# Optimization experiments

Measured on AMD Instinct MI355X. Metric: run time of the kernel, lower is better.

The kernel has to match this reference:

```python
import jax, jax.numpy as jnp
import numpy as np

N_HEAD = 16
D_MODEL = 1024
T_DIM = 64
# Faithful to torch source: temperature = d_model // n_head ** 0.5  ==  d_model // (n_head**0.5)
TEMPERATURE = D_MODEL // (N_HEAD ** 0.5)  # 1024 // 4.0 = 256.0
LN_EPS = 1e-5


def setup_inputs() -> dict:
    key = jax.random.key(0)
    ks = jax.random.split(key, 10)
    B, S = 4, 2048
    w = 0.02  # weight scale to keep activations/logits in a sane range
    return {
        "q": jax.random.normal(ks[0], (B, S, D_MODEL), jnp.float32),
        "k": jax.random.normal(ks[1], (B, S, D_MODEL), jnp.float32),
        "v": jax.random.normal(ks[2], (B, S, D_MODEL), jnp.float32),
        "t": jax.random.normal(ks[3], (B, T_DIM), jnp.float32),
        "w_q": jax.random.normal(ks[4], (D_MODEL, D_MODEL), jnp.float32) * w,
        "w_k": jax.random.normal(ks[5], (D_MODEL, D_MODEL), jnp.float32) * w,
        "w_v": jax.random.normal(ks[6], (D_MODEL, D_MODEL), jnp.float32) * w,
        "w_fc": jax.random.normal(ks[7], (D_MODEL, D_MODEL), jnp.float32) * w,
        "ada_w": jax.random.normal(ks[8], (2 * D_MODEL, T_DIM), jnp.float32) * w,
        "ada_b": jax.random.normal(ks[9], (2 * D_MODEL,), jnp.float32) * w,
    }


def _ada_layer_norm(x, t_emb, ada_w, ada_b):
    # linear(gelu(t_emb)) -> [B, 2*d]; exact (erf) GELU as in torch nn.GELU default
    emb = jax.nn.gelu(t_emb, approximate=False) @ ada_w.T + ada_b
    emb = emb[:, None, :]  # [B, 1, 2*d]
    scale, shift = jnp.split(emb, 2, axis=-1)
    mean = jnp.mean(x, axis=-1, keepdims=True)
    var = jnp.var(x, axis=-1, keepdims=True)
    ln = (x - mean) * jax.lax.rsqrt(var + LN_EPS)
    return ln * (1.0 + scale) + shift


def reference(q, k, v, t, w_q, w_k, w_v, w_fc, ada_w, ada_b):
    B, Sq, D = q.shape
    Sk = k.shape[1]
    H, Dk = N_HEAD, D // N_HEAD

    q = _ada_layer_norm(q, t, ada_w, ada_b)
    residual = q

    # projections (torch Linear, no bias): y = x @ W.T
    qh = (q @ w_q.T).reshape(B, Sq, H, Dk).transpose(0, 2, 1, 3)  # [B,H,Sq,Dk]
    kh = (k @ w_k.T).reshape(B, Sk, H, Dk).transpose(0, 2, 1, 3)
    vh = (v @ w_v.T).reshape(B, Sk, H, Dk).transpose(0, 2, 1, 3)

    scores = jnp.einsum("bhqd,bhkd->bhqk", qh, kh) / TEMPERATURE
    attn = jax.nn.softmax(scores, axis=-1)
    out = jnp.einsum("bhqk,bhkd->bhqd", attn, vh)  # [B,H,Sq,Dk]

    out = out.transpose(0, 2, 1, 3).reshape(B, Sq, D)
    out = out @ w_fc.T  # dropout is identity in eval
    return out + residual
```

## Files before the change

### kernel.cpp

```cpp
#include <hip/hip_runtime.h>
#include <hip/hip_bf16.h>
#include <cstdint>

typedef short bf16x8 __attribute__((ext_vector_type(8)));
typedef float f32x4  __attribute__((ext_vector_type(4)));
typedef unsigned short u16x8 __attribute__((ext_vector_type(8)));
typedef unsigned short u16x4 __attribute__((ext_vector_type(4)));

#define SEQ    2048
#define BATCH  4
#define DMODEL 1024
#define NHEAD  16
#define DKH    64
#define MROWS  (BATCH * SEQ)

__device__ __forceinline__ unsigned short f2bf(float f) {
  union { float f; uint32_t u; } x; x.f = f;
  uint32_t r = (x.u + 0x7fffu + ((x.u >> 16) & 1u)) >> 16;
  return (unsigned short)r;
}
__device__ __forceinline__ float bf2f(unsigned short u) {
  union { uint32_t u; float f; } x; x.u = ((uint32_t)u) << 16;
  return x.f;
}
__device__ __forceinline__ uint32_t pack_bf2(float lo, float hi) {
  uint32_t r;
  asm("v_cvt_pk_bf16_f32 %0, %1, %2" : "=v"(r) : "v"(lo), "v"(hi));
  return r;
}
__device__ __forceinline__ void gload_lds16(const void* g, void* l) {
  __builtin_amdgcn_global_load_lds(
      (const __attribute__((address_space(1))) void*)g,
      (__attribute__((address_space(3))) void*)l, 16, 0, 0);
}

__global__ __launch_bounds__(256) void cast4_kernel(
    const float* __restrict__ s0, const float* __restrict__ s1,
    const float* __restrict__ s2, const float* __restrict__ s3,
    unsigned short* __restrict__ d0, unsigned short* __restrict__ d1,
    unsigned short* __restrict__ d2, unsigned short* __restrict__ d3) {
  int z = blockIdx.y;
  const float* in = z == 0 ? s0 : z == 1 ? s1 : z == 2 ? s2 : s3;
  unsigned short* out = z == 0 ? d0 : z == 1 ? d1 : z == 2 ? d2 : d3;
  int i = (blockIdx.x * 256 + threadIdx.x) * 4;
  float4 v = *(const float4*)(in + i);
  u16x4 o;
  o[0] = f2bf(v.x); o[1] = f2bf(v.y); o[2] = f2bf(v.z); o[3] = f2bf(v.w);
  *(u16x4*)(out + i) = o;
}

__global__ __launch_bounds__(256) void cast2_kernel(
    const float* __restrict__ s0, const float* __restrict__ s1,
    unsigned short* __restrict__ d0, unsigned short* __restrict__ d1) {
  int z = blockIdx.y;
  const float* in = z == 0 ? s0 : s1;
  unsigned short* out = z == 0 ? d0 : d1;
  int i = (blockIdx.x * 256 + threadIdx.x) * 4;
  float4 v = *(const float4*)(in + i);
  u16x4 o;
  o[0] = f2bf(v.x); o[1] = f2bf(v.y); o[2] = f2bf(v.z); o[3] = f2bf(v.w);
  *(u16x4*)(out + i) = o;
}

__global__ __launch_bounds__(256) void ada_emb_kernel(
    const float* __restrict__ t, const float* __restrict__ ada_w,
    const float* __restrict__ ada_b, float* __restrict__ emb) {
  int b = blockIdx.y;
  int j = blockIdx.x * 256 + threadIdx.x;
  __shared__ float g[64];
  if (threadIdx.x < 64) {
    float x = t[b * 64 + threadIdx.x];
    g[threadIdx.x] = x * 0.5f * (1.0f + erff(x * 0.70710678118654752f));
  }
  __syncthreads();
  float acc = ada_b[j];
  const float* wr = ada_w + (size_t)j * 64;
  #pragma unroll
  for (int i = 0; i < 64; ++i) acc += g[i] * wr[i];
  emb[b * 2048 + j] = acc;
}

__global__ __launch_bounds__(256) void adaln_kernel(
    const float* __restrict__ q, const float* __restrict__ emb,
    unsigned short* __restrict__ xbf) {
  int row = blockIdx.x;
  int b = row >> 11;
  int tid = threadIdx.x;
  float4 x = ((const float4*)(q + (size_t)row * DMODEL))[tid];
  float s  = x.x + x.y + x.z + x.w;
  float s2 = x.x * x.x + x.y * x.y + x.z * x.z + x.w * x.w;
  #pragma unroll
  for (int off = 32; off > 0; off >>= 1) {
    s  += __shfl_down(s, off);
    s2 += __shfl_down(s2, off);
  }
  __shared__ float red[8];
  int w = tid >> 6;
  if ((tid & 63) == 0) { red[w * 2] = s; red[w * 2 + 1] = s2; }
  __syncthreads();
  s  = red[0] + red[2] + red[4] + red[6];
  s2 = red[1] + red[3] + red[5] + red[7];
  float mean = s * (1.0f / 1024.0f);
  float var  = s2 * (1.0f / 1024.0f) - mean * mean;
  float rs = rsqrtf(var + 1e-5f);
  float4 sc = ((const float4*)(emb + (size_t)b * 2048))[tid];
  float4 sh = ((const float4*)(emb + (size_t)b * 2048 + 1024))[tid];
  u16x4 o;
  o[0] = f2bf((x.x - mean) * rs * (1.0f + sc.x) + sh.x);
  o[1] = f2bf((x.y - mean) * rs * (1.0f + sc.y) + sh.y);
  o[2] = f2bf((x.z - mean) * rs * (1.0f + sc.z) + sh.z);
  o[3] = f2bf((x.w - mean) * rs * (1.0f + sc.w) + sh.w);
  ((u16x4*)(xbf + (size_t)row * DMODEL))[tid] = o;
}

template <int MODE>
__device__ __forceinline__ void gemm_body(
    const unsigned short* A, const unsigned short* Bw,
    unsigned short* Cb, const unsigned short* resid, float* Cf) {
  __shared__ __align__(16) unsigned short Al[128 * 64];
  __shared__ __align__(16) unsigned short Bl[128 * 64];
  int tid = threadIdx.x;
  int lane = tid & 63, w = tid >> 6;
  int l15 = lane & 15, l16 = lane >> 4;
  int m0 = blockIdx.y * 128, n0 = blockIdx.x * 128;
  int wr = w >> 1, wc = w & 1;

  f32x4 acc[4][4];
  #pragma unroll
  for (int m = 0; m < 4; ++m)
    #pragma unroll
    for (int n = 0; n < 4; ++n) acc[m][n] = {0.f, 0.f, 0.f, 0.f};

  const unsigned short* Ab = A + (size_t)m0 * 1024;
  const unsigned short* Bb = Bw + (size_t)n0 * 1024;

  for (int kt = 0; kt < 16; ++kt) {
    int k0 = kt * 64;
    #pragma unroll
    for (int it = 0; it < 4; ++it) {
      int c = it * 256 + tid;
      int r = c >> 3, cg = c & 7;
      gload_lds16(Ab + (size_t)r * 1024 + k0 + cg * 8, &Al[c * 8]);
    }
    #pragma unroll
    for (int it = 0; it < 4; ++it) {
      int c = it * 256 + tid;
      int r = c >> 3, cg = c & 7;
      gload_lds16(Bb + (size_t)r * 1024 + k0 + cg * 8, &Bl[c * 8]);
    }
    __syncthreads();
    #pragma unroll
    for (int kk = 0; kk < 2; ++kk) {
      bf16x8 af[4], bfr[4];
      #pragma unroll
      for (int m = 0; m < 4; ++m)
        af[m] = *(const bf16x8*)&Al[(wr * 64 + m * 16 + l15) * 64 + kk * 32 + l16 * 8];
      #pragma unroll
      for (int n = 0; n < 4; ++n)
        bfr[n] = *(const bf16x8*)&Bl[(wc * 64 + n * 16 + l15) * 64 + kk * 32 + l16 * 8];
      __builtin_amdgcn_s_setprio(1);
      #pragma unroll
      for (int m = 0; m < 4; ++m)
        #pragma unroll
        for (int n = 0; n < 4; ++n)
          acc[m][n] = __builtin_amdgcn_mfma_f32_16x16x32_bf16(af[m], bfr[n], acc[m][n], 0, 0, 0);
      __builtin_amdgcn_s_setprio(0);
    }
    __syncthreads();
  }

  #pragma unroll
  for (int m = 0; m < 4; ++m) {
    #pragma unroll
    for (int r = 0; r < 4; ++r) {
      int row = m0 + wr * 64 + m * 16 + l16 * 4 + r;
      size_t base = (size_t)row * 1024 + n0 + wc * 64 + l15;
      #pragma unroll
      for (int n = 0; n < 4; ++n) {
        float val = acc[m][n][r];
        if (MODE == 0) {
          Cb[base + n * 16] = f2bf(val);
        } else {
          Cf[base + n * 16] = val + bf2f(resid[base + n * 16]);
        }
      }
    }
  }
}

__global__ __launch_bounds__(256) void gemm_qkv_kernel(
    const unsigned short* xbf, const unsigned short* kbf, const unsigned short* vbf,
    const unsigned short* wq, const unsigned short* wk, const unsigned short* wv,
    unsigned short* qh, unsigned short* kh, unsigned short* vh) {
  int z = blockIdx.z;
  const unsigned short* A = z == 0 ? xbf : z == 1 ? kbf : vbf;
  const unsigned short* B = z == 0 ? wq  : z == 1 ? wk  : wv;
  unsigned short* C       = z == 0 ? qh  : z == 1 ? kh  : vh;
  gemm_body<0>(A, B, C, nullptr, nullptr);
}

__global__ __launch_bounds__(256) void gemm_fc_kernel(
    const unsigned short* attn, const unsigned short* wfc,
    const unsigned short* resid, float* outf) {
  gemm_body<1>(attn, wfc, nullptr, resid, outf);
}

__global__ __launch_bounds__(256) void attn_kernel(
    const unsigned short* __restrict__ Q, const unsigned short* __restrict__ K,
    const unsigned short* __restrict__ V, unsigned short* __restrict__ O) {
  int tid = threadIdx.x;
  int lane = tid & 63, w = tid >> 6;
  int l15 = lane & 15, l16 = lane >> 4;
  int sw7 = l15 & 7;

  int wgid = blockIdx.x;
  int e = (wgid & 7) * 128 + (wgid >> 3);
  int qt = e & 15, h = (e >> 4) & 15, b = e >> 8;

  __shared__ __align__(16) unsigned short Kl[64 * 64];
  __shared__ __align__(16) unsigned short VT[64 * 64];
  __shared__ __align__(16) unsigned short Pl[4][16 * 64];

  size_t hb = (size_t)b * SEQ * DMODEL + (size_t)h * DKH;
  int qrow = qt * 128 + w * 32;

  bf16x8 qf[2][2];
  #pragma unroll
  for (int qs = 0; qs < 2; ++qs)
    #pragma unroll
    for (int kk = 0; kk < 2; ++kk)
      qf[qs][kk] = *(const bf16x8*)(Q + hb + (size_t)(qrow + qs * 16 + l15) * DMODEL + kk * 32 + l16 * 8);

  const float csc = 1.44269504f / 256.0f;
  const float THR = 1280.0f;

  float m_s[2]  = {-INFINITY, -INFINITY};
  float mc_s[2] = {-INFINITY, -INFINITY};
  float l_s[2]  = {0.f, 0.f};
  f32x4 oacc[2][4];
  #pragma unroll
  for (int qs = 0; qs < 2; ++qs)
    #pragma unroll
    for (int mm = 0; mm < 4; ++mm) oacc[qs][mm] = {0.f, 0.f, 0.f, 0.f};

  for (int t = 0; t < SEQ / 64; ++t) {
    int kv0 = t * 64;
    #pragma unroll
    for (int it = 0; it < 2; ++it) {
      int c = it * 256 + tid;
      int r = c >> 3, cg = c & 7;
      gload_lds16(K + hb + (size_t)(kv0 + r) * DMODEL + (cg ^ (r & 7)) * 8, &Kl[c * 8]);
    }
    {
      int kv = lane, dk0 = w * 16;
      const unsigned short* vp = V + hb + (size_t)(kv0 + kv) * DMODEL + dk0;
      u16x8 v0 = *(const u16x8*)vp;
      u16x8 v1 = *(const u16x8*)(vp + 8);
      int kvhi = kv >> 3, kvlo = kv & 7;
      #pragma unroll
      for (int e2 = 0; e2 < 8; ++e2) {
        int d = dk0 + e2;
        VT[d * 64 + ((kvhi ^ (d & 7)) << 3) + kvlo] = v0[e2];
      }
      #pragma unroll
      for (int e2 = 0; e2 < 8; ++e2) {
        int d = dk0 + 8 + e2;
        VT[d * 64 + ((kvhi ^ (d & 7)) << 3) + kvlo] = v1[e2];
      }
    }
    __syncthreads();

    bf16x8 kf[2][4], vf[2][4];
    #pragma unroll
    for (int kk = 0; kk < 2; ++kk)
      #pragma unroll
      for (int n = 0; n < 4; ++n)
        kf[kk][n] = *(const bf16x8*)&Kl[(n * 16 + l15) * 64 + (((kk * 4 + l16) ^ sw7) << 3)];
    #pragma unroll
    for (int kk = 0; kk < 2; ++kk)
      #pragma unroll
      for (int mm = 0; mm < 4; ++mm)
        vf[kk][mm] = *(const bf16x8*)&VT[(mm * 16 + l15) * 64 + (((kk * 4 + l16) ^ sw7) << 3)];

    #pragma unroll
    for (int qs = 0; qs < 2; ++qs) {
      f32x4 sa[4];
      #pragma unroll
      for (int n = 0; n < 4; ++n) sa[n] = {0.f, 0.f, 0.f, 0.f};
      __builtin_amdgcn_s_setprio(1);
      #pragma unroll
      for (int kk = 0; kk < 2; ++kk)
        #pragma unroll
        for (int n = 0; n < 4; ++n)
          sa[n] = __builtin_amdgcn_mfma_f32_16x16x32_bf16(kf[kk][n], qf[qs][kk], sa[n], 0, 0, 0);
      __builtin_amdgcn_s_setprio(0);

      float pmax = fmaxf(fmaxf(fmaxf(sa[0][0], sa[0][1]), fmaxf(sa[0][2], sa[0][3])),
                         fmaxf(fmaxf(sa[1][0], sa[1][1]), fmaxf(sa[1][2], sa[1][3])));
      pmax = fmaxf(pmax, fmaxf(fmaxf(fmaxf(sa[2][0], sa[2][1]), fmaxf(sa[2][2], sa[2][3])),
                               fmaxf(fmaxf(sa[3][0], sa[3][1]), fmaxf(sa[3][2], sa[3][3]))));
      pmax = fmaxf(pmax, __shfl_xor(pmax, 16));
      pmax = fmaxf(pmax, __shfl_xor(pmax, 32));
      if (!__all(pmax - m_s[qs] <= THR)) {
        float mn = fmaxf(m_s[qs], pmax);
        float corr = __builtin_exp2f((m_s[qs] - mn) * csc);
        m_s[qs] = mn;
        mc_s[qs] = mn * csc;
        l_s[qs] *= corr;
        #pragma unroll
        for (int mm = 0; mm < 4; ++mm)
          #pragma unroll
          for (int r = 0; r < 4; ++r) oacc[qs][mm][r] *= corr;
      }
      float mc = mc_s[qs];
      float rsum = 0.f;
      #pragma unroll
      for (int n = 0; n < 4; ++n)
        #pragma unroll
        for (int r = 0; r < 4; ++r) {
          sa[n][r] = __builtin_exp2f(__builtin_fmaf(sa[n][r], csc, -mc));
          rsum += sa[n][r];
        }
      rsum += __shfl_xor(rsum, 16);
      rsum += __shfl_xor(rsum, 32);
      l_s[qs] += rsum;

      #pragma unroll
      for (int n = 0; n < 4; ++n) {
        #pragma unroll
        for (int r0 = 0; r0 < 4; r0 += 2) {
          uint32_t pw = pack_bf2(sa[n][r0], sa[n][r0 + 1]);
          int idx = l15 * 64 + (((n * 2 + (l16 >> 1)) ^ sw7) << 3) + (l16 & 1) * 4 + r0;
          *(uint32_t*)&Pl[w][idx] = pw;
        }
      }
      bf16x8 pf[2];
      #pragma unroll
      for (int kk = 0; kk < 2; ++kk)
        pf[kk] = *(const bf16x8*)&Pl[w][l15 * 64 + (((kk * 4 + l16) ^ sw7) << 3)];

      __builtin_amdgcn_s_setprio(1);
      #pragma unroll
      for (int kk = 0; kk < 2; ++kk)
        #pragma unroll
        for (int mm = 0; mm < 4; ++mm)
          oacc[qs][mm] = __builtin_amdgcn_mfma_f32_16x16x32_bf16(vf[kk][mm], pf[kk], oacc[qs][mm], 0, 0, 0);
      __builtin_amdgcn_s_setprio(0);
    }
    __syncthreads();
  }

  #pragma unroll
  for (int qs = 0; qs < 2; ++qs) {
    float inv = 1.0f / l_s[qs];
    #pragma unroll
    for (int mm = 0; mm < 4; ++mm) {
      uint32_t w0 = pack_bf2(oacc[qs][mm][0] * inv, oacc[qs][mm][1] * inv);
      uint32_t w1 = pack_bf2(oacc[qs][mm][2] * inv, oacc[qs][mm][3] * inv);
      uint2 ov = {w0, w1};
      *(uint2*)(O + hb + (size_t)(qrow + qs * 16 + l15) * DMODEL + mm * 16 + l16 * 4) = ov;
    }
  }
}

static constexpr size_t EMB_OFF = 0;
static constexpr size_t WQ_OFF  = 32768;
static constexpr size_t WK_OFF  = WQ_OFF + 2097152;
static constexpr size_t WV_OFF  = WK_OFF + 2097152;
static constexpr size_t WFC_OFF = WV_OFF + 2097152;
static constexpr size_t XBF_OFF = WFC_OFF + 2097152;
static constexpr size_t KBF_OFF = XBF_OFF + 16777216;
static constexpr size_t VBF_OFF = KBF_OFF + 16777216;
static constexpr size_t QH_OFF  = VBF_OFF + 16777216;
static constexpr size_t KH_OFF  = QH_OFF + 16777216;
static constexpr size_t VH_OFF  = KH_OFF + 16777216;
static constexpr size_t ATTN_OFF = KBF_OFF;

extern "C" void kernel_launch(void* const* d_in, const int* in_sizes, int n_in,
                              void* d_out, int out_size, void* d_ws, size_t ws_size,
                              hipStream_t stream) {
  const float* q     = (const float*)d_in[0];
  const float* k     = (const float*)d_in[1];
  const float* v     = (const float*)d_in[2];
  const float* t     = (const float*)d_in[3];
  const float* w_q   = (const float*)d_in[4];
  const float* w_k   = (const float*)d_in[5];
  const float* w_v   = (const float*)d_in[6];
  const float* w_fc  = (const float*)d_in[7];
  const float* ada_w = (const float*)d_in[8];
  const float* ada_b = (const float*)d_in[9];

  char* ws = (char*)d_ws;
  float* emb           = (float*)(ws + EMB_OFF);
  unsigned short* wqb  = (unsigned short*)(ws + WQ_OFF);
  unsigned short* wkb  = (unsigned short*)(ws + WK_OFF);
  unsigned short* wvb  = (unsigned short*)(ws + WV_OFF);
  unsigned short* wfcb = (unsigned short*)(ws + WFC_OFF);
  unsigned short* xbf  = (unsigned short*)(ws + XBF_OFF);
  unsigned short* kbf  = (unsigned short*)(ws + KBF_OFF);
  unsigned short* vbf  = (unsigned short*)(ws + VBF_OFF);
  unsigned short* qh   = (unsigned short*)(ws + QH_OFF);
  unsigned short* kh   = (unsigned short*)(ws + KH_OFF);
  unsigned short* vh   = (unsigned short*)(ws + VH_OFF);
  unsigned short* attn = (unsigned short*)(ws + ATTN_OFF);
  float* outf          = (float*)d_out;

  cast4_kernel<<<dim3(1024, 4), 256, 0, stream>>>(w_q, w_k, w_v, w_fc, wqb, wkb, wvb, wfcb);
  cast2_kernel<<<dim3(8192, 2), 256, 0, stream>>>(k, v, kbf, vbf);

  ada_emb_kernel<<<dim3(8, 4), 256, 0, stream>>>(t, ada_w, ada_b, emb);

  adaln_kernel<<<8192, 256, 0, stream>>>(q, emb, xbf);

  gemm_qkv_kernel<<<dim3(8, 64, 3), 256, 0, stream>>>(xbf, kbf, vbf, wqb, wkb, wvb, qh, kh, vh);

  attn_kernel<<<1024, 256, 0, stream>>>(qh, kh, vh, attn);

  gemm_fc_kernel<<<dim3(8, 64), 256, 0, stream>>>(attn, wfcb, xbf, outf);
}
```

Baseline: 435.7 us.

## Double-buffer K/V tiles in attention with prefetch and a single barrier

The attention kernel now double-buffers the K and transposed-V LDS tiles. The next tile's K global-to-LDS loads and V register loads are issued right after the barrier, so they overlap the current tile's MFMA and softmax work, and the trailing barrier per iteration is removed. It also adds launch_bounds occupancy hint 4 and unroll 2. The cost is doubled LDS for K and V and extra registers for the prefetched V, which could reduce occupancy. The full vmcnt(0) wait before the barrier also forces the prefetch to finish each iteration.

```diff
diff --git a/kernel.cpp b/kernel.cpp
--- a/kernel.cpp
+++ b/kernel.cpp
@@ -205,7 +205,7 @@
   gemm_body<1>(attn, wfc, nullptr, resid, outf);
 }
 
-__global__ __launch_bounds__(256) void attn_kernel(
+__global__ __launch_bounds__(256, 4) void attn_kernel(
     const unsigned short* __restrict__ Q, const unsigned short* __restrict__ K,
     const unsigned short* __restrict__ V, unsigned short* __restrict__ O) {
   int tid = threadIdx.x;
@@ -217,8 +217,8 @@
   int e = (wgid & 7) * 128 + (wgid >> 3);
   int qt = e & 15, h = (e >> 4) & 15, b = e >> 8;
 
-  __shared__ __align__(16) unsigned short Kl[64 * 64];
-  __shared__ __align__(16) unsigned short VT[64 * 64];
+  __shared__ __align__(16) unsigned short Kl[2][64 * 64];
+  __shared__ __align__(16) unsigned short VT[2][64 * 64];
   __shared__ __align__(16) unsigned short Pl[4][16 * 64];
 
   size_t hb = (size_t)b * SEQ * DMODEL + (size_t)h * DKH;
@@ -243,44 +243,62 @@
     #pragma unroll
     for (int mm = 0; mm < 4; ++mm) oacc[qs][mm] = {0.f, 0.f, 0.f, 0.f};
 
-  for (int t = 0; t < SEQ / 64; ++t) {
-    int kv0 = t * 64;
-    #pragma unroll
-    for (int it = 0; it < 2; ++it) {
-      int c = it * 256 + tid;
-      int r = c >> 3, cg = c & 7;
-      gload_lds16(K + hb + (size_t)(kv0 + r) * DMODEL + (cg ^ (r & 7)) * 8, &Kl[c * 8]);
-    }
-    {
-      int kv = lane, dk0 = w * 16;
-      const unsigned short* vp = V + hb + (size_t)(kv0 + kv) * DMODEL + dk0;
-      u16x8 v0 = *(const u16x8*)vp;
-      u16x8 v1 = *(const u16x8*)(vp + 8);
-      int kvhi = kv >> 3, kvlo = kv & 7;
-      #pragma unroll
-      for (int e2 = 0; e2 < 8; ++e2) {
-        int d = dk0 + e2;
-        VT[d * 64 + ((kvhi ^ (d & 7)) << 3) + kvlo] = v0[e2];
+  const unsigned short* vbase = V + hb + (size_t)lane * DMODEL + w * 16;
+  int kvhi = lane >> 3, kvlo = lane & 7;
+  int dk0 = w * 16;
+
+  #pragma unroll
+  for (int it = 0; it < 2; ++it) {
+    int c = it * 256 + tid;
+    int r = c >> 3, cg = c & 7;
+    gload_lds16(K + hb + (size_t)r * DMODEL + (cg ^ (r & 7)) * 8, &Kl[0][c * 8]);
+  }
+  u16x8 vr0 = *(const u16x8*)vbase;
+  u16x8 vr1 = *(const u16x8*)(vbase + 8);
+
+  #pragma unroll 2
+  for (int t = 0; t < 32; ++t) {
+    int cur = t & 1, nxt = cur ^ 1;
+
+    #pragma unroll
+    for (int e2 = 0; e2 < 8; ++e2) {
+      int d = dk0 + e2;
+      VT[cur][d * 64 + ((kvhi ^ (d & 7)) << 3) + kvlo] = vr0[e2];
+    }
+    #pragma unroll
+    for (int e2 = 0; e2 < 8; ++e2) {
+      int d = dk0 + 8 + e2;
+      VT[cur][d * 64 + ((kvhi ^ (d & 7)) << 3) + kvlo] = vr1[e2];
+    }
+
+    asm volatile("s_waitcnt vmcnt(0) lgkmcnt(0)" ::: "memory");
+    __builtin_amdgcn_s_barrier();
+    __builtin_amdgcn_sched_barrier(0);
+
+    if (t + 1 < 32) {
+      int kv0n = (t + 1) * 64;
+      #pragma unroll
+      for (int it = 0; it < 2; ++it) {
+        int c = it * 256 + tid;
+        int r = c >> 3, cg = c & 7;
+        gload_lds16(K + hb + (size_t)(kv0n + r) * DMODEL + (cg ^ (r & 7)) * 8, &Kl[nxt][c * 8]);
       }
-      #pragma unroll
-      for (int e2 = 0; e2 < 8; ++e2) {
-        int d = dk0 + 8 + e2;
-        VT[d * 64 + ((kvhi ^ (d & 7)) << 3) + kvlo] = v1[e2];
-      }
-    }
-    __syncthreads();
+      const unsigned short* vp = vbase + (size_t)kv0n * DMODEL;
+      vr0 = *(const u16x8*)vp;
+      vr1 = *(const u16x8*)(vp + 8);
+    }
 
     bf16x8 kf[2][4], vf[2][4];
     #pragma unroll
     for (int kk = 0; kk < 2; ++kk)
       #pragma unroll
       for (int n = 0; n < 4; ++n)
-        kf[kk][n] = *(const bf16x8*)&Kl[(n * 16 + l15) * 64 + (((kk * 4 + l16) ^ sw7) << 3)];
+        kf[kk][n] = *(const bf16x8*)&Kl[cur][(n * 16 + l15) * 64 + (((kk * 4 + l16) ^ sw7) << 3)];
     #pragma unroll
     for (int kk = 0; kk < 2; ++kk)
       #pragma unroll
       for (int mm = 0; mm < 4; ++mm)
-        vf[kk][mm] = *(const bf16x8*)&VT[(mm * 16 + l15) * 64 + (((kk * 4 + l16) ^ sw7) << 3)];
+        vf[kk][mm] = *(const bf16x8*)&VT[cur][(mm * 16 + l15) * 64 + (((kk * 4 + l16) ^ sw7) << 3)];
 
     #pragma unroll
     for (int qs = 0; qs < 2; ++qs) {
@@ -347,7 +365,6 @@
           oacc[qs][mm] = __builtin_amdgcn_mfma_f32_16x16x32_bf16(vf[kk][mm], pf[kk], oacc[qs][mm], 0, 0, 0);
       __builtin_amdgcn_s_setprio(0);
     }
-    __syncthreads();
   }
 
   #pragma unroll
```

After: 793.8 us. +82.2%, slower.
